# Performance work log

Hardware: AMD Instinct MI355X
Metric: run time of the kernel (lower is better)

## Reference

```python
import jax, jax.numpy as jnp
import numpy as np

B, C, H, W = 16, 64, 64, 64

def setup_inputs() -> dict:
    key = jax.random.key(0)
    k1, k2, k3, k4, k5 = jax.random.split(key, 5)
    x = jax.random.normal(k1, (B, C, H, W), dtype=jnp.float32)
    w1 = jax.random.normal(k2, (C // 2, C), dtype=jnp.float32) * (1.0 / np.sqrt(C))
    w2 = jax.random.normal(k3, (C // 2, C), dtype=jnp.float32) * (1.0 / np.sqrt(C))
    w3 = jax.random.normal(k4, (C, C), dtype=jnp.float32) * (1.0 / np.sqrt(C))
    gamma = jax.random.normal(k5, (1,), dtype=jnp.float32)
    return {"x": x, "w1": w1, "w2": w2, "w3": w3, "gamma": gamma}

def reference(x, w1, w2, w3, gamma):
    b, c, h, w = x.shape
    n = h * w
    xf = x.reshape(b, c, n)                      # [B, C, N] (1x1 conv == channel matmul)
    c1 = jnp.einsum('dc,bcn->bdn', w1, xf)       # [B, C/2, N]
    c2 = jnp.einsum('dc,bcn->bdn', w2, xf)       # [B, C/2, N]
    c3 = jnp.einsum('oc,bcn->bon', w3, xf)       # [B, C, N]
    # matrix[b,i,j] = sum_d c2[b,d,i] * c1[b,d,j]
    matrix = jnp.einsum('bdi,bdj->bij', c2, c1)  # [B, N, N]
    attention = jax.nn.softmax(matrix, axis=-1)  # softmax over last dim
    # refined[b,c,k] = sum_j c3[b,c,j] * attention[b,k,j]
    refined = jnp.einsum('bcj,bkj->bck', c3, attention)  # [B, C, N]
    refined = refined.reshape(b, c, h, w)
    return gamma[0] * refined + x
```

## Files before the change

kernel.cpp:

```cpp
#include <hip/hip_runtime.h>
#include <hip/hip_bf16.h>

#define Bn 16
#define Nn 4096

typedef __attribute__((ext_vector_type(8))) short bf16x8;
typedef __attribute__((ext_vector_type(16))) float f32x16;

static __device__ __forceinline__ unsigned short f2bf(float f) {
    union { float f; unsigned int u; } v; v.f = f;
    return (unsigned short)((v.u + 0x7fffu + ((v.u >> 16) & 1u)) >> 16);
}
static __device__ __forceinline__ int cvtpk(float lo, float hi) {
    int d; asm("v_cvt_pk_bf16_f32 %0, %1, %2" : "=v"(d) : "v"(lo), "v"(hi)); return d;
}
static __device__ __forceinline__ bf16x8 mkfrag(int a, int b, int c, int d) {
    union { int i[4]; bf16x8 v; } u; u.i[0]=a; u.i[1]=b; u.i[2]=c; u.i[3]=d; return u.v;
}

__global__ __launch_bounds__(256) void qkv_kernel(
    const float* __restrict__ x,
    const float* __restrict__ w1,
    const float* __restrict__ w2,
    const float* __restrict__ w3,
    uint4* __restrict__ Qf,
    uint4* __restrict__ Kf,
    uint4* __restrict__ Vf)
{
    __shared__ float wlds[128 * 64];
    __shared__ __align__(16) unsigned short vtile[64][136];

    const int t = threadIdx.x;
    {
        float4* wd = (float4*)wlds;
        const float4* s1 = (const float4*)w1;
        const float4* s2 = (const float4*)w2;
        const float4* s3 = (const float4*)w3;
        wd[t]       = s1[t];
        wd[256 + t] = s1[256 + t];
        wd[512 + t] = s2[t];
        wd[768 + t] = s2[256 + t];
        #pragma unroll
        for (int k = 0; k < 4; ++k) wd[1024 + k * 256 + t] = s3[k * 256 + t];
    }

    const int half = t >> 7;
    const int nl = t & 127;
    const int b = blockIdx.x >> 5;
    const int n = ((blockIdx.x & 31) << 7) + nl;
    const float* xb = x + ((size_t)b << 18) + n;
    float xr[64];
    #pragma unroll
    for (int c = 0; c < 64; ++c) xr[c] = xb[(size_t)c << 12];

    __syncthreads();

    if (half == 0) {
        const int ntile = ((blockIdx.x & 31) << 2) + (nl >> 5);
        #pragma unroll
        for (int sel = 0; sel < 2; ++sel) {
            const float* wbase = wlds + sel * 2048;
            uint4* dst = (sel ? Qf : Kf) + (((size_t)b * 128 + ntile) * 2) * 64;
            #pragma unroll
            for (int dt = 0; dt < 2; ++dt) {
                float acc[16];
                #pragma unroll
                for (int i = 0; i < 16; ++i) {
                    const float* wr = wbase + (dt * 16 + i) * 64;
                    float a = 0.f;
                    #pragma unroll
                    for (int c4 = 0; c4 < 16; ++c4) {
                        const float4 wv = *(const float4*)(wr + c4 * 4);
                        a = fmaf(wv.x, xr[c4 * 4 + 0], a);
                        a = fmaf(wv.y, xr[c4 * 4 + 1], a);
                        a = fmaf(wv.z, xr[c4 * 4 + 2], a);
                        a = fmaf(wv.w, xr[c4 * 4 + 3], a);
                    }
                    acc[i] = a;
                }
                uint4 u0, u1;
                u0.x = (unsigned)f2bf(acc[0])  | ((unsigned)f2bf(acc[1])  << 16);
                u0.y = (unsigned)f2bf(acc[2])  | ((unsigned)f2bf(acc[3])  << 16);
                u0.z = (unsigned)f2bf(acc[4])  | ((unsigned)f2bf(acc[5])  << 16);
                u0.w = (unsigned)f2bf(acc[6])  | ((unsigned)f2bf(acc[7])  << 16);
                u1.x = (unsigned)f2bf(acc[8])  | ((unsigned)f2bf(acc[9])  << 16);
                u1.y = (unsigned)f2bf(acc[10]) | ((unsigned)f2bf(acc[11]) << 16);
                u1.z = (unsigned)f2bf(acc[12]) | ((unsigned)f2bf(acc[13]) << 16);
                u1.w = (unsigned)f2bf(acc[14]) | ((unsigned)f2bf(acc[15]) << 16);
                dst[(size_t)dt * 64 + (nl & 31)]      = u0;
                dst[(size_t)dt * 64 + 32 + (nl & 31)] = u1;
            }
        }
    } else {
        #pragma unroll
        for (int dg = 0; dg < 8; ++dg) {
            #pragma unroll
            for (int i = 0; i < 8; ++i) {
                const float* wr = wlds + (64 + dg * 8 + i) * 64;
                float a = 0.f;
                #pragma unroll
                for (int c4 = 0; c4 < 16; ++c4) {
                    const float4 wv = *(const float4*)(wr + c4 * 4);
                    a = fmaf(wv.x, xr[c4 * 4 + 0], a);
                    a = fmaf(wv.y, xr[c4 * 4 + 1], a);
                    a = fmaf(wv.z, xr[c4 * 4 + 2], a);
                    a = fmaf(wv.w, xr[c4 * 4 + 3], a);
                }
                vtile[dg * 8 + i][nl] = f2bf(a);
            }
        }
    }
    __syncthreads();

    #pragma unroll
    for (int i = 0; i < 4; ++i) {
        const int slot = t * 4 + i;
        const int l   = slot & 63;
        const int jt  = (slot >> 6) & 1;
        const int ct  = (slot >> 7) & 1;
        const int kvt = slot >> 8;
        const int row  = ct * 32 + (l & 31);
        const int base = kvt * 32 + jt * 16 + ((l >> 5) << 2);
        const uint2 lo = *(const uint2*)&vtile[row][base];
        const uint2 hi = *(const uint2*)&vtile[row][base + 8];
        const int kvtg = ((blockIdx.x & 31) << 2) + kvt;
        Vf[((((size_t)b * 128 + kvtg) * 2 + ct) * 2 + jt) * 64 + l] =
            make_uint4(lo.x, lo.y, hi.x, hi.y);
    }
}

__global__ __launch_bounds__(512) void attn_kernel(
    const bf16x8* __restrict__ Qf,
    const bf16x8* __restrict__ Kf,
    const bf16x8* __restrict__ Vf,
    const float* __restrict__ x,
    const float* __restrict__ gamma,
    float* __restrict__ out)
{
    __shared__ __align__(16) unsigned char kvbuf[2 * 12288];
    __shared__ float mgbuf[4 * 64 * 37];

    const int t    = threadIdx.x;
    const int lane = t & 63;
    const int wv   = t >> 6;
    const int id   = blockIdx.x;
    const int b    = 2 * (id & 7) + ((id >> 3) >> 5);
    const int qg   = (id >> 3) & 31;
    const int qt   = qg * 4 + (wv & 3);
    const int h    = wv >> 2;

    const bf16x8* Qp = Qf + ((size_t)(b * 128 + qt) * 2) * 64;
    const bf16x8  qf0 = Qp[lane];
    const bf16x8  qf1 = Qp[64 + lane];
    const bf16x8* Kp = Kf + (size_t)b * 128 * 2 * 64;
    const bf16x8* Vp = Vf + (size_t)b * 128 * 4 * 64;

    const int s0  = (t >= 384);
    const int r0  = t - s0 * 384;
    const int sl0 = r0 >> 6;
    const int l0  = r0 & 63;
    const int dof0 = s0 * 12288 + r0 * 16;
    const bool two = (t < 256);
    const int r1  = t + 128;
    const int sl1 = r1 >> 6;
    const int l1  = t & 63;
    const int dof1 = 12288 + r1 * 16;

    #define SRC_OF(SLOT, S, NX, LN)                                              \
        ((SLOT) < 2 ? (Kp + ((size_t)((S) * 64 + (NX)) * 2 + (SLOT)) * 64 + (LN)) \
                    : (Vp + ((size_t)((S) * 64 + (NX)) * 4 + ((SLOT) - 2)) * 64 + (LN)))

    {
        uint4 st0 = *(const uint4*)SRC_OF(sl0, s0, 0, l0);
        uint4 st1 = two ? *(const uint4*)SRC_OF(sl1, 1, 0, l1) : make_uint4(0, 0, 0, 0);
        *(uint4*)(kvbuf + dof0) = st0;
        if (two) *(uint4*)(kvbuf + dof1) = st1;
    }
    __syncthreads();

    f32x16 o0 = {}, o1 = {};
    float lacc = 0.f;

    for (int i = 0; i < 64; ++i) {
        uint4 st0, st1;
        if (i < 63) {
            st0 = *(const uint4*)SRC_OF(sl0, s0, i + 1, l0);
            if (two) st1 = *(const uint4*)SRC_OF(sl1, 1, i + 1, l1);
        }

        const bf16x8* bc = (const bf16x8*)(kvbuf + h * 12288 + (i & 1) * 6144);
        const bf16x8 kf0 = bc[lane];
        const bf16x8 kf1 = bc[64 + lane];
        const bf16x8 v00 = bc[128 + lane];
        const bf16x8 v01 = bc[192 + lane];
        const bf16x8 v10 = bc[256 + lane];
        const bf16x8 v11 = bc[320 + lane];

        f32x16 s;
        {
            f32x16 z = {};
            s = __builtin_amdgcn_mfma_f32_32x32x16_bf16(kf0, qf0, z, 0, 0, 0);
            s = __builtin_amdgcn_mfma_f32_32x32x16_bf16(kf1, qf1, s, 0, 0, 0);
        }

        float p[16];
        #pragma unroll
        for (int j = 0; j < 16; ++j) p[j] = __expf(s[j]);
        float b0 = (p[0] + p[1]) + (p[2] + p[3]);
        float b1 = (p[4] + p[5]) + (p[6] + p[7]);
        float b2 = (p[8] + p[9]) + (p[10] + p[11]);
        float b3 = (p[12] + p[13]) + (p[14] + p[15]);
        lacc += (b0 + b1) + (b2 + b3);

        const bf16x8 pf0 = mkfrag(cvtpk(p[0],  p[1]),  cvtpk(p[2],  p[3]),
                                  cvtpk(p[4],  p[5]),  cvtpk(p[6],  p[7]));
        const bf16x8 pf1 = mkfrag(cvtpk(p[8],  p[9]),  cvtpk(p[10], p[11]),
                                  cvtpk(p[12], p[13]), cvtpk(p[14], p[15]));

        o0 = __builtin_amdgcn_mfma_f32_32x32x16_bf16(v00, pf0, o0, 0, 0, 0);
        o0 = __builtin_amdgcn_mfma_f32_32x32x16_bf16(v01, pf1, o0, 0, 0, 0);
        o1 = __builtin_amdgcn_mfma_f32_32x32x16_bf16(v10, pf0, o1, 0, 0, 0);
        o1 = __builtin_amdgcn_mfma_f32_32x32x16_bf16(v11, pf1, o1, 0, 0, 0);

        if (i < 63) {
            const int bo = ((i + 1) & 1) * 6144;
            *(uint4*)(kvbuf + dof0 + bo) = st0;
            if (two) *(uint4*)(kvbuf + dof1 + bo) = st1;
        }
        __syncthreads();
    }
    #undef SRC_OF

    if (wv >= 4) {
        float* mg = mgbuf + ((size_t)(wv - 4) * 64 + lane) * 37;
        #pragma unroll
        for (int j = 0; j < 16; ++j) { mg[j] = o0[j]; mg[16 + j] = o1[j]; }
        mg[32] = lacc;
    }
    __syncthreads();
    if (wv < 4) {
        const float* mg = mgbuf + ((size_t)wv * 64 + lane) * 37;
        #pragma unroll
        for (int j = 0; j < 16; ++j) { o0[j] += mg[j]; o1[j] += mg[16 + j]; }
        lacc += mg[32];

        const float g = gamma[0];
        const float lt = lacc + __shfl_xor(lacc, 32, 64);
        const float rl = 1.0f / lt;
        const int n = qt * 32 + (lane & 31);
        const int hi1 = lane >> 5;
        #pragma unroll
        for (int r = 0; r < 16; ++r) {
            const int c0r = (r & 3) + 8 * (r >> 2) + 4 * hi1;
            {
                const size_t idx = (((size_t)b * 64 + c0r) << 12) + n;
                out[idx] = g * o0[r] * rl + x[idx];
            }
            {
                const size_t idx = (((size_t)b * 64 + 32 + c0r) << 12) + n;
                out[idx] = g * o1[r] * rl + x[idx];
            }
        }
    }
}

extern "C" void kernel_launch(void* const* d_in, const int* in_sizes, int n_in,
                              void* d_out, int out_size, void* d_ws, size_t ws_size,
                              hipStream_t stream) {
    const float* x     = (const float*)d_in[0];
    const float* w1    = (const float*)d_in[1];
    const float* w2    = (const float*)d_in[2];
    const float* w3    = (const float*)d_in[3];
    const float* gamma = (const float*)d_in[4];
    float* out = (float*)d_out;

    uint4* Qf = (uint4*)d_ws;
    uint4* Kf = Qf + (size_t)Bn * 128 * 2 * 64;
    uint4* Vf = Kf + (size_t)Bn * 128 * 2 * 64;

    qkv_kernel<<<512, 256, 0, stream>>>(x, w1, w2, w3, Qf, Kf, Vf);
    attn_kernel<<<512, 512, 0, stream>>>((const bf16x8*)Qf, (const bf16x8*)Kf,
                                         (const bf16x8*)Vf, x, gamma, out);
}
```

Baseline: 109.5 us.

## Split attention KV range across four wave groups with 1024-thread blocks

Each attention block now runs 16 waves, four KV-split groups of four query tiles each, instead of two groups. Every group walks 32 KV tiles instead of 64, sharing one double-buffered LDS staging area. The partial outputs and row sums are merged by a serial three-step reduction through LDS that reuses the KV buffer. This shortens the per-block serial loop and adds warps for latency hiding, at the cost of more barriers, a larger reduction, and possible register pressure at 1024 threads.

```diff
diff --git a/kernel.cpp b/kernel.cpp
--- a/kernel.cpp
+++ b/kernel.cpp
@@ -129,7 +129,7 @@
     }
 }
 
-__global__ __launch_bounds__(512) void attn_kernel(
+__global__ __launch_bounds__(1024) void attn_kernel(
     const bf16x8* __restrict__ Qf,
     const bf16x8* __restrict__ Kf,
     const bf16x8* __restrict__ Vf,
@@ -137,8 +137,7 @@
     const float* __restrict__ gamma,
     float* __restrict__ out)
 {
-    __shared__ __align__(16) unsigned char kvbuf[2 * 12288];
-    __shared__ float mgbuf[4 * 64 * 37];
+    __shared__ __align__(16) unsigned char kvbuf[4 * 2 * 6144];
 
     const int t    = threadIdx.x;
     const int lane = t & 63;
@@ -155,24 +154,26 @@
     const bf16x8* Kp = Kf + (size_t)b * 128 * 2 * 64;
     const bf16x8* Vp = Vf + (size_t)b * 128 * 4 * 64;
 
-    const int s0  = (t >= 384);
+    const int s0  = t / 384;
     const int r0  = t - s0 * 384;
     const int sl0 = r0 >> 6;
     const int l0  = r0 & 63;
     const int dof0 = s0 * 12288 + r0 * 16;
-    const bool two = (t < 256);
-    const int r1  = t + 128;
+    const bool two = (t < 512);
+    const int c1  = 1024 + t;
+    const int s1  = c1 / 384;
+    const int r1  = c1 - s1 * 384;
     const int sl1 = r1 >> 6;
-    const int l1  = t & 63;
-    const int dof1 = 12288 + r1 * 16;
-
-    #define SRC_OF(SLOT, S, NX, LN)                                              \
-        ((SLOT) < 2 ? (Kp + ((size_t)((S) * 64 + (NX)) * 2 + (SLOT)) * 64 + (LN)) \
-                    : (Vp + ((size_t)((S) * 64 + (NX)) * 4 + ((SLOT) - 2)) * 64 + (LN)))
+    const int l1  = r1 & 63;
+    const int dof1 = s1 * 12288 + r1 * 16;
+
+    #define SRC_OF(SLOT, S, NX, LN)                                               \
+        ((SLOT) < 2 ? (Kp + ((size_t)((S) * 32 + (NX)) * 2 + (SLOT)) * 64 + (LN))  \
+                    : (Vp + ((size_t)((S) * 32 + (NX)) * 4 + ((SLOT) - 2)) * 64 + (LN)))
 
     {
         uint4 st0 = *(const uint4*)SRC_OF(sl0, s0, 0, l0);
-        uint4 st1 = two ? *(const uint4*)SRC_OF(sl1, 1, 0, l1) : make_uint4(0, 0, 0, 0);
+        uint4 st1 = two ? *(const uint4*)SRC_OF(sl1, s1, 0, l1) : make_uint4(0, 0, 0, 0);
         *(uint4*)(kvbuf + dof0) = st0;
         if (two) *(uint4*)(kvbuf + dof1) = st1;
     }
@@ -181,11 +182,11 @@
     f32x16 o0 = {}, o1 = {};
     float lacc = 0.f;
 
-    for (int i = 0; i < 64; ++i) {
+    for (int i = 0; i < 32; ++i) {
         uint4 st0, st1;
-        if (i < 63) {
+        if (i < 31) {
             st0 = *(const uint4*)SRC_OF(sl0, s0, i + 1, l0);
-            if (two) st1 = *(const uint4*)SRC_OF(sl1, 1, i + 1, l1);
+            if (two) st1 = *(const uint4*)SRC_OF(sl1, s1, i + 1, l1);
         }
 
         const bf16x8* bc = (const bf16x8*)(kvbuf + h * 12288 + (i & 1) * 6144);
@@ -222,7 +223,7 @@
         o1 = __builtin_amdgcn_mfma_f32_32x32x16_bf16(v10, pf0, o1, 0, 0, 0);
         o1 = __builtin_amdgcn_mfma_f32_32x32x16_bf16(v11, pf1, o1, 0, 0, 0);
 
-        if (i < 63) {
+        if (i < 31) {
             const int bo = ((i + 1) & 1) * 6144;
             *(uint4*)(kvbuf + dof0 + bo) = st0;
             if (two) *(uint4*)(kvbuf + dof1 + bo) = st1;
@@ -231,19 +232,24 @@
     }
     #undef SRC_OF
 
-    if (wv >= 4) {
-        float* mg = mgbuf + ((size_t)(wv - 4) * 64 + lane) * 37;
-        #pragma unroll
-        for (int j = 0; j < 16; ++j) { mg[j] = o0[j]; mg[16 + j] = o1[j]; }
-        mg[32] = lacc;
-    }
-    __syncthreads();
-    if (wv < 4) {
-        const float* mg = mgbuf + ((size_t)wv * 64 + lane) * 37;
-        #pragma unroll
-        for (int j = 0; j < 16; ++j) { o0[j] += mg[j]; o1[j] += mg[16 + j]; }
-        lacc += mg[32];
-
+    float* mrow = (float*)kvbuf + ((size_t)((wv & 3) * 64 + lane)) * 33;
+    #pragma unroll 1
+    for (int g = 1; g < 4; ++g) {
+        if (h == g) {
+            #pragma unroll
+            for (int j = 0; j < 16; ++j) { mrow[j] = o0[j]; mrow[16 + j] = o1[j]; }
+            mrow[32] = lacc;
+        }
+        __syncthreads();
+        if (h == 0) {
+            #pragma unroll
+            for (int j = 0; j < 16; ++j) { o0[j] += mrow[j]; o1[j] += mrow[16 + j]; }
+            lacc += mrow[32];
+        }
+        __syncthreads();
+    }
+
+    if (h == 0) {
         const float g = gamma[0];
         const float lt = lacc + __shfl_xor(lacc, 32, 64);
         const float rl = 1.0f / lt;
@@ -279,6 +285,6 @@
     uint4* Vf = Kf + (size_t)Bn * 128 * 2 * 64;
 
     qkv_kernel<<<512, 256, 0, stream>>>(x, w1, w2, w3, Qf, Kf, Vf);
-    attn_kernel<<<512, 512, 0, stream>>>((const bf16x8*)Qf, (const bf16x8*)Kf,
-                                         (const bf16x8*)Vf, x, gamma, out);
-}
+    attn_kernel<<<512, 1024, 0, stream>>>((const bf16x8*)Qf, (const bf16x8*)Kf,
+                                          (const bf16x8*)Vf, x, gamma, out);
+}
```

Measured after the change: 112.2 us. 2.4% more time.
